# Kernel tuning notes

Hardware: AMD Instinct MI355X
Metric: run time of the kernel (lower is better)

## Reference

```python
import jax, jax.numpy as jnp
import numpy as np

NUM_HEADS = 16
HEAD_DIM = 80
HIDDEN = 1280
SEQ = 3072
NUM_SEGS = 6  # 6 packed images of 512 patches each


def rotate_half(x):
    x1, x2 = jnp.split(x, 2, axis=-1)
    return jnp.concatenate([-x2, x1], axis=-1)


def setup_inputs() -> dict:
    key = jax.random.key(0)
    ks = jax.random.split(key, 6)
    hidden_states = jax.random.normal(ks[0], (SEQ, HIDDEN), dtype=jnp.float32)
    # RoPE tables as in Qwen-VL vision: freqs over half the head_dim, duplicated
    half = HEAD_DIM // 2
    inv_freq = 1.0 / (10000.0 ** (jnp.arange(half, dtype=jnp.float32) / half))
    pos = jnp.arange(SEQ, dtype=jnp.float32)[:, None]
    freqs = pos * inv_freq[None, :]                      # (SEQ, half)
    emb = jnp.concatenate([freqs, freqs], axis=-1)       # (SEQ, HEAD_DIM)
    cos = jnp.cos(emb)
    sin = jnp.sin(emb)
    # Packed segment boundaries: [0, 512, 1024, ..., 3072]
    cu_seqlens = jnp.arange(0, SEQ + 1, SEQ // NUM_SEGS, dtype=jnp.int32)
    scale = 0.02
    w_qkv = jax.random.normal(ks[1], (3 * HIDDEN, HIDDEN), dtype=jnp.float32) * scale
    b_qkv = jax.random.normal(ks[2], (3 * HIDDEN,), dtype=jnp.float32) * scale
    w_proj = jax.random.normal(ks[3], (HIDDEN, HIDDEN), dtype=jnp.float32) * scale
    b_proj = jax.random.normal(ks[4], (HIDDEN,), dtype=jnp.float32) * scale
    return {
        "hidden_states": hidden_states, "cos": cos, "sin": sin,
        "w_qkv": w_qkv, "b_qkv": b_qkv, "w_proj": w_proj, "b_proj": b_proj,
        "cu_seqlens": cu_seqlens,
    }


def reference(hidden_states, cos, sin, w_qkv, b_qkv, w_proj, b_proj, cu_seqlens):
    S, H = hidden_states.shape
    nh, hd = NUM_HEADS, H // NUM_HEADS

    # Fused QKV projection: (S, 3H) -> q, k, v each (S, nh, hd)
    qkv = hidden_states @ w_qkv.T + b_qkv
    qkv = qkv.reshape(S, 3, nh, hd)
    q, k, v = qkv[:, 0], qkv[:, 1], qkv[:, 2]

    # Inline RoPE on q/k (cos/sin broadcast over heads)
    c = cos[:, None, :]
    s = sin[:, None, :]
    q = q * c + rotate_half(q) * s
    k = k * c + rotate_half(k) * s

    # Original casts fp32 -> fp16 for the flash attention kernel
    q16 = q.astype(jnp.float16)
    k16 = k.astype(jnp.float16)
    v16 = v.astype(jnp.float16)

    # Varlen masking: tokens attend only within their own packed segment
    tok = jnp.arange(S)
    seg = jnp.searchsorted(cu_seqlens, tok, side="right")  # (S,)
    same_seg = seg[:, None] == seg[None, :]                 # (S, S)

    scale = hd ** (-0.5)
    # Scores accumulated in fp32 (as flash attention does internally)
    scores = jnp.einsum("qhd,khd->hqk", q16, k16,
                        preferred_element_type=jnp.float32) * scale
    scores = jnp.where(same_seg[None], scores, jnp.finfo(jnp.float32).min)
    weights = jax.nn.softmax(scores, axis=-1).astype(jnp.float16)  # (nh, S, S)

    attn = jnp.einsum("hqk,khd->qhd", weights, v16)  # (S, nh, hd) fp16
    attn = attn.astype(jnp.float32).reshape(S, H)
    return attn @ w_proj.T + b_proj
```

## Files before the change

### kernel.cpp

```cpp
#include <hip/hip_runtime.h>

typedef _Float16 f16;
typedef _Float16 half8 __attribute__((ext_vector_type(8)));
typedef _Float16 half4 __attribute__((ext_vector_type(4)));
typedef float f32x4 __attribute__((ext_vector_type(4)));

__device__ __forceinline__ void gld_lds16(const void* g, void* l) {
  __builtin_amdgcn_global_load_lds((const __attribute__((address_space(1))) void*)g,
                                   (__attribute__((address_space(3))) void*)l, 16, 0, 0);
}

template <int CTRL>
__device__ __forceinline__ float dppf(float x) {
  return __builtin_bit_cast(float,
      __builtin_amdgcn_mov_dpp(__builtin_bit_cast(int, x), CTRL, 0xf, 0xf, true));
}
__device__ __forceinline__ float dpp_max16(float v) {
  v = fmaxf(v, dppf<0xB1>(v));
  v = fmaxf(v, dppf<0x4E>(v));
  v = fmaxf(v, dppf<0x128>(v));
  v = fmaxf(v, dppf<0x140>(v));
  return v;
}
__device__ __forceinline__ float dpp_sum16(float v) {
  v += dppf<0xB1>(v);
  v += dppf<0x4E>(v);
  v += dppf<0x128>(v);
  v += dppf<0x140>(v);
  return v;
}

__global__ void cvt_all(const float* __restrict__ hid, const float* __restrict__ wq,
                        const float* __restrict__ wp, f16* __restrict__ hid16,
                        f16* __restrict__ wq16, f16* __restrict__ wp16) {
  int b = blockIdx.x;
  const float* in;
  f16* out;
  int i;
  if (b < 3840) { in = hid; out = hid16; i = b * 256 + threadIdx.x; }
  else if (b < 8640) { in = wq; out = wq16; i = (b - 3840) * 256 + threadIdx.x; }
  else { in = wp; out = wp16; i = (b - 8640) * 256 + threadIdx.x; }
  float4 v = ((const float4*)in)[i];
  half4 o;
  o.x = (f16)v.x; o.y = (f16)v.y; o.z = (f16)v.z; o.w = (f16)v.w;
  ((half4*)out)[i] = o;
}

__global__ __launch_bounds__(512, 2) void gemm256(const f16* __restrict__ A,
                                                  const f16* __restrict__ B,
                                                  const float* __restrict__ bias,
                                                  f16* __restrict__ C) {
  __shared__ f16 S[65536];
  char* Sb = (char*)S;
  const int tid = threadIdx.x, lane = tid & 63, wid = tid >> 6;
  const int lm = lane & 15, q4 = lane >> 4;
  const int wm = wid >> 2, wn = wid & 3;
  const int bm = blockIdx.x * 256, bn = blockIdx.y * 256;
  const int w2 = wid * 2048;

  const int ch = ((lane & 7) ^ (lane >> 3)) << 3;
  const int r0 = wid * 16 + (lane >> 3);
  const int r1 = r0 + 8;
  uint32_t aoff[2][2], boff[2][2];
#pragma unroll
  for (int h = 0; h < 2; h++) {
    aoff[h][0] = (uint32_t)((bm + h * 64 + (r0 & 63) + ((r0 >> 6) << 7)) * 1280 + ch);
    aoff[h][1] = (uint32_t)((bm + h * 64 + (r1 & 63) + ((r1 >> 6) << 7)) * 1280 + ch);
    boff[h][0] = (uint32_t)((bn + h * 32 + (r0 & 31) + ((r0 >> 5) << 6)) * 1280 + ch);
    boff[h][1] = (uint32_t)((bn + h * 32 + (r1 & 31) + ((r1 >> 5) << 6)) * 1280 + ch);
  }

  int aro[4][2], bro[2][2];
#pragma unroll
  for (int f = 0; f < 4; f++)
#pragma unroll
    for (int ks = 0; ks < 2; ks++) {
      int row = wm * 64 + f * 16 + lm, colb = ks * 64 + q4 * 16;
      aro[f][ks] = row * 128 + (colb ^ ((row & 7) << 4));
    }
#pragma unroll
  for (int j = 0; j < 2; j++)
#pragma unroll
    for (int ks = 0; ks < 2; ks++) {
      int row = wn * 32 + j * 16 + lm, colb = ks * 64 + q4 * 16;
      bro[j][ks] = row * 128 + (colb ^ ((row & 7) << 4));
    }

  f32x4 acc[8][4] = {};

  {
    char* A0 = Sb;
    char* B0 = Sb + 65536;
    char* A1 = Sb + 32768;
    char* B1 = Sb + 98304;
    gld_lds16(A + aoff[0][0], A0 + w2);
    gld_lds16(A + aoff[0][1], A0 + w2 + 1024);
    gld_lds16(B + boff[1][0], B0 + 16384 + w2);
    gld_lds16(B + boff[1][1], B0 + 16384 + w2 + 1024);
    gld_lds16(A + aoff[1][0], A0 + 16384 + w2);
    gld_lds16(A + aoff[1][1], A0 + 16384 + w2 + 1024);
    gld_lds16(B + boff[0][0], B0 + w2);
    gld_lds16(B + boff[0][1], B0 + w2 + 1024);
    gld_lds16(A + aoff[0][0] + 64, A1 + w2);
    gld_lds16(A + aoff[0][1] + 64, A1 + w2 + 1024);
    gld_lds16(B + boff[1][0] + 64, B1 + 16384 + w2);
    gld_lds16(B + boff[1][1] + 64, B1 + 16384 + w2 + 1024);
    gld_lds16(A + aoff[1][0] + 64, A1 + 16384 + w2);
    gld_lds16(A + aoff[1][1] + 64, A1 + 16384 + w2 + 1024);
    asm volatile("s_waitcnt vmcnt(6)" ::: "memory");
    __builtin_amdgcn_s_barrier();
  }

  constexpr int NT = 20;
  half8 af[4][2], bf[2][2];
  for (int t = 0; t < NT; ++t) {
    const int p = t & 1;
    char* Ab = Sb + p * 32768;
    char* Bb = Sb + 65536 + p * 32768;
    char* Bn = Sb + 65536 + (p ^ 1) * 32768;
    const int k1 = (t + 1 < NT ? t + 1 : NT - 1) * 64;
    const int k2 = (t + 2 < NT ? t + 2 : NT - 1) * 64;

#pragma unroll
    for (int f = 0; f < 4; f++) {
      af[f][0] = *(const half8*)(Ab + aro[f][0]);
      af[f][1] = *(const half8*)(Ab + aro[f][1]);
    }
#pragma unroll
    for (int j = 0; j < 2; j++) {
      bf[j][0] = *(const half8*)(Bb + bro[j][0]);
      bf[j][1] = *(const half8*)(Bb + bro[j][1]);
    }
    gld_lds16(B + boff[0][0] + k1, Bn + w2);
    gld_lds16(B + boff[0][1] + k1, Bn + w2 + 1024);
    __builtin_amdgcn_s_barrier();
    asm volatile("s_waitcnt lgkmcnt(0)" ::: "memory");
    __builtin_amdgcn_sched_barrier(0);
    __builtin_amdgcn_s_setprio(1);
#pragma unroll
    for (int ks = 0; ks < 2; ks++)
#pragma unroll
      for (int f = 0; f < 4; f++)
#pragma unroll
        for (int j = 0; j < 2; j++)
          acc[f][j] =
              __builtin_amdgcn_mfma_f32_16x16x32_f16(af[f][ks], bf[j][ks], acc[f][j], 0, 0, 0);
    __builtin_amdgcn_s_setprio(0);
    __builtin_amdgcn_s_barrier();

#pragma unroll
    for (int j = 0; j < 2; j++) {
      bf[j][0] = *(const half8*)(Bb + 16384 + bro[j][0]);
      bf[j][1] = *(const half8*)(Bb + 16384 + bro[j][1]);
    }
    gld_lds16(A + aoff[0][0] + k2, Ab + w2);
    gld_lds16(A + aoff[0][1] + k2, Ab + w2 + 1024);
    __builtin_amdgcn_s_barrier();
    asm volatile("s_waitcnt lgkmcnt(0)" ::: "memory");
    __builtin_amdgcn_sched_barrier(0);
    __builtin_amdgcn_s_setprio(1);
#pragma unroll
    for (int ks = 0; ks < 2; ks++)
#pragma unroll
      for (int f = 0; f < 4; f++)
#pragma unroll
        for (int j = 0; j < 2; j++)
          acc[f][2 + j] =
              __builtin_amdgcn_mfma_f32_16x16x32_f16(af[f][ks], bf[j][ks], acc[f][2 + j], 0, 0, 0);
    __builtin_amdgcn_s_setprio(0);
    __builtin_amdgcn_s_barrier();

#pragma unroll
    for (int f = 0; f < 4; f++) {
      af[f][0] = *(const half8*)(Ab + 16384 + aro[f][0]);
      af[f][1] = *(const half8*)(Ab + 16384 + aro[f][1]);
    }
    gld_lds16(B + boff[1][0] + k2, Bb + 16384 + w2);
    gld_lds16(B + boff[1][1] + k2, Bb + 16384 + w2 + 1024);
    __builtin_amdgcn_s_barrier();
    asm volatile("s_waitcnt lgkmcnt(0)" ::: "memory");
    __builtin_amdgcn_sched_barrier(0);
    __builtin_amdgcn_s_setprio(1);
#pragma unroll
    for (int ks = 0; ks < 2; ks++)
#pragma unroll
      for (int f = 0; f < 4; f++)
#pragma unroll
        for (int j = 0; j < 2; j++)
          acc[4 + f][2 + j] = __builtin_amdgcn_mfma_f32_16x16x32_f16(af[f][ks], bf[j][ks],
                                                                     acc[4 + f][2 + j], 0, 0, 0);
    __builtin_amdgcn_s_setprio(0);
    __builtin_amdgcn_s_barrier();

#pragma unroll
    for (int j = 0; j < 2; j++) {
      bf[j][0] = *(const half8*)(Bb + bro[j][0]);
      bf[j][1] = *(const half8*)(Bb + bro[j][1]);
    }
    gld_lds16(A + aoff[1][0] + k2, Ab + 16384 + w2);
    gld_lds16(A + aoff[1][1] + k2, Ab + 16384 + w2 + 1024);
    asm volatile("s_waitcnt vmcnt(6)" ::: "memory");
    __builtin_amdgcn_s_barrier();
    asm volatile("s_waitcnt lgkmcnt(0)" ::: "memory");
    __builtin_amdgcn_sched_barrier(0);
    __builtin_amdgcn_s_setprio(1);
#pragma unroll
    for (int ks = 0; ks < 2; ks++)
#pragma unroll
      for (int f = 0; f < 4; f++)
#pragma unroll
        for (int j = 0; j < 2; j++)
          acc[4 + f][j] =
              __builtin_amdgcn_mfma_f32_16x16x32_f16(af[f][ks], bf[j][ks], acc[4 + f][j], 0, 0, 0);
    __builtin_amdgcn_s_setprio(0);
    __builtin_amdgcn_s_barrier();
  }

#pragma unroll
  for (int mf = 0; mf < 8; mf++)
#pragma unroll
    for (int nf = 0; nf < 4; nf++) {
      const int gc = bn + wn * 64 + nf * 16 + lm;
      const float bb = bias[gc];
      const int gr0 = bm + wm * 128 + mf * 16 + q4 * 4;
#pragma unroll
      for (int r = 0; r < 4; r++)
        C[(size_t)(gr0 + r) * 3840 + gc] = (f16)(acc[mf][nf][r] + bb);
    }
}

template <bool OUT_F16>
__global__ __launch_bounds__(256, 2) void gemm_bt64(const f16* __restrict__ A,
                                                    const f16* __restrict__ B,
                                                    const float* __restrict__ bias,
                                                    void* __restrict__ Cout,
                                                    int K, int lda, int ldb, int ldc) {
  __shared__ f16 As[64 * 32];
  __shared__ f16 Bs[128 * 32];
  const int tid = threadIdx.x, lane = tid & 63, wave = tid >> 6;
  const int bm = blockIdx.x * 64, bn = blockIdx.y * 128;
  const int wm = (wave & 1) * 32, wn = (wave >> 1) * 64;
  const int lm = lane & 15, kq = (lane >> 4) * 8;
  const int arow = tid >> 2, acol = (tid & 3) * 8;

  const f16* Ab = A + (size_t)(bm + arow) * lda + acol;
  const f16* Bb = B + (size_t)(bn + arow) * ldb + acol;
  f16* AsW = As + wave * 512;
  f16* BsW = Bs + wave * 512;

  f32x4 acc[2][4] = {};
  for (int k0 = 0; k0 < K; k0 += 32) {
    gld_lds16(Ab + k0, AsW);
    gld_lds16(Bb + k0, BsW);
    gld_lds16(Bb + (size_t)64 * ldb + k0, BsW + 2048);
    __syncthreads();
    half8 af[2], bf[4];
#pragma unroll
    for (int mt = 0; mt < 2; mt++) af[mt] = *(const half8*)&As[(wm + 16 * mt + lm) * 32 + kq];
#pragma unroll
    for (int nt = 0; nt < 4; nt++) bf[nt] = *(const half8*)&Bs[(wn + 16 * nt + lm) * 32 + kq];
#pragma unroll
    for (int mt = 0; mt < 2; mt++)
#pragma unroll
      for (int nt = 0; nt < 4; nt++)
        acc[mt][nt] = __builtin_amdgcn_mfma_f32_16x16x32_f16(af[mt], bf[nt], acc[mt][nt], 0, 0, 0);
    __syncthreads();
  }
  const int q4 = lane >> 4;
#pragma unroll
  for (int mt = 0; mt < 2; mt++)
#pragma unroll
    for (int nt = 0; nt < 4; nt++)
#pragma unroll
      for (int r = 0; r < 4; r++) {
        int gr = bm + wm + 16 * mt + 4 * q4 + r;
        int gc = bn + wn + 16 * nt + lm;
        float v = acc[mt][nt][r] + bias[gc];
        if (OUT_F16)
          ((f16*)Cout)[(size_t)gr * ldc + gc] = (f16)v;
        else
          ((float*)Cout)[(size_t)gr * ldc + gc] = v;
      }
}

__global__ void rope_transpose(f16* __restrict__ qkv, const float* __restrict__ cosb,
                               const float* __restrict__ sinb, f16* __restrict__ vt) {
  __shared__ f16 tile[64][72];
  const int b = blockIdx.x;
  if (b < 1920) {
    int idx = b * 256 + threadIdx.x;
    int c = idx % 5;
    int t = idx / 5;
    int h = t % 16; t /= 16;
    int qk = t & 1;
    int s = t >> 1;
    size_t base = (size_t)s * 3840 + qk * 1280 + h * 80 + c * 8;
    half8 x = *(half8*)&qkv[base];
    half8 y = *(half8*)&qkv[base + 40];
    const float* cp = cosb + s * 80 + c * 8;
    const float* sp = sinb + s * 80 + c * 8;
    half8 ox, oy;
#pragma unroll
    for (int i = 0; i < 8; i++) {
      float cs = cp[i], sn = sp[i];
      float xf = (float)x[i], yf = (float)y[i];
      ox[i] = (f16)(xf * cs - yf * sn);
      oy[i] = (f16)(yf * cs + xf * sn);
    }
    *(half8*)&qkv[base] = ox;
    *(half8*)&qkv[base + 40] = oy;
  } else {
    const int bb = b - 1920;
    const int bs = (bb % 48) * 64;
    const int bd = (bb / 48) * 64;
    const int r = threadIdx.x >> 2, c = (threadIdx.x & 3) * 16;
    *(uint4*)&tile[r][c] = *(const uint4*)&qkv[(size_t)(bs + r) * 3840 + 2560 + bd + c];
    *(uint4*)&tile[r][c + 8] = *(const uint4*)&qkv[(size_t)(bs + r) * 3840 + 2560 + bd + c + 8];
    __syncthreads();
    f16 tmp[16];
#pragma unroll
    for (int i = 0; i < 16; i++) tmp[i] = tile[c + i][r];
    *(uint4*)&vt[(size_t)(bd + r) * 3072 + bs + c] = *(uint4*)&tmp[0];
    *(uint4*)&vt[(size_t)(bd + r) * 3072 + bs + c + 8] = *(uint4*)&tmp[8];
  }
}

__global__ __launch_bounds__(256, 4) void flash_attn5(const f16* __restrict__ qkv,
                                                      const f16* __restrict__ vt,
                                                      f16* __restrict__ attn) {
  __shared__ f16 S[20480];
  f16* Ks = S;
  f16* Vs = S + 10240;
  const int tid = threadIdx.x, lane = tid & 63, wave = tid >> 6;
  const int lm = lane & 15, q4 = lane >> 4;
  const int h = blockIdx.x, g = blockIdx.z;
  const int qbase = g * 512 + blockIdx.y * 64 + wave * 16;
  f16* P = S + wave * 2112;
  const half8 hz = {};

  const f16* qrow = qkv + (size_t)(qbase + lm) * 3840 + h * 80;
  half8 qf[3];
  qf[0] = *(const half8*)(qrow + q4 * 8);
  qf[1] = *(const half8*)(qrow + 32 + q4 * 8);
  qf[2] = (q4 < 2) ? *(const half8*)(qrow + 64 + q4 * 8) : hz;

  size_t kgo[5], vgo[5];
#pragma unroll
  for (int i = 0; i < 5; i++) {
    int t = (wave * 5 + i) * 1024 + lane * 16;
    int kr = t / 160, kcb = t % 160;
    kgo[i] = (size_t)(g * 512 + kr) * 3840 + 1280 + h * 80 + (kcb >> 1);
    int vd = t >> 8, vsb = t & 255;
    vgo[i] = (size_t)(h * 80 + vd) * 3072 + g * 512 + (vsb >> 1);
  }

  f32x4 oacc[5] = {};
  float mprev[4] = {-1e30f, -1e30f, -1e30f, -1e30f};
  float lsum[4] = {0.f, 0.f, 0.f, 0.f};
  const float sc = 0.11180339887498949f * 1.4426950408889634f;

  for (int j = 0; j < 4; j++) {
    __syncthreads();
#pragma unroll
    for (int i = 0; i < 5; i++) {
      int chunk = wave * 5 + i;
      gld_lds16(qkv + kgo[i] + (size_t)j * (128 * 3840), Ks + chunk * 512);
      gld_lds16(vt + vgo[i] + j * 128, Vs + chunk * 512);
    }
    __syncthreads();

    f32x4 sacc[8] = {};
#pragma unroll
    for (int ks = 0; ks < 3; ks++) {
      half8 bk[8];
#pragma unroll
      for (int nt = 0; nt < 8; nt++)
        bk[nt] = (ks < 2 || q4 < 2)
                     ? *(const half8*)&Ks[(16 * nt + lm) * 80 + 32 * ks + q4 * 8]
                     : hz;
#pragma unroll
      for (int nt = 0; nt < 8; nt++)
        sacc[nt] = __builtin_amdgcn_mfma_f32_16x16x32_f16(qf[ks], bk[nt], sacc[nt], 0, 0, 0);
    }

    float mnew[4], alpha[4], rs[4];
#pragma unroll
    for (int r = 0; r < 4; r++) {
      float v = fmaxf(fmaxf(fmaxf(sacc[0][r], sacc[1][r]), fmaxf(sacc[2][r], sacc[3][r])),
                      fmaxf(fmaxf(sacc[4][r], sacc[5][r]), fmaxf(sacc[6][r], sacc[7][r])));
      v = dpp_max16(v);
      mnew[r] = fmaxf(mprev[r], v * sc);
      alpha[r] = __builtin_exp2f(mprev[r] - mnew[r]);
      mprev[r] = mnew[r];
      rs[r] = 0.f;
    }
#pragma unroll
    for (int nt = 0; nt < 8; nt++)
#pragma unroll
      for (int r = 0; r < 4; r++) {
        float p = __builtin_exp2f(sacc[nt][r] * sc - mnew[r]);
        sacc[nt][r] = p;
        rs[r] += p;
      }
#pragma unroll
    for (int r = 0; r < 4; r++) {
      float v = dpp_sum16(rs[r]);
      lsum[r] = alpha[r] * lsum[r] + v;
#pragma unroll
      for (int nt2 = 0; nt2 < 5; nt2++) oacc[nt2][r] *= alpha[r];
    }

    __syncthreads();
#pragma unroll
    for (int nt = 0; nt < 8; nt++)
#pragma unroll
      for (int r = 0; r < 4; r++)
        P[(4 * q4 + r) * 132 + 16 * nt + lm] = (f16)sacc[nt][r];

#pragma unroll
    for (int ks = 0; ks < 4; ks++) {
      half8 ap = *(const half8*)&P[lm * 132 + ks * 32 + q4 * 8];
      half8 bv[5];
#pragma unroll
      for (int nt2 = 0; nt2 < 5; nt2++)
        bv[nt2] = *(const half8*)&Vs[(16 * nt2 + lm) * 128 + ks * 32 + q4 * 8];
#pragma unroll
      for (int nt2 = 0; nt2 < 5; nt2++)
        oacc[nt2] = __builtin_amdgcn_mfma_f32_16x16x32_f16(ap, bv[nt2], oacc[nt2], 0, 0, 0);
    }
  }
#pragma unroll
  for (int r = 0; r < 4; r++) {
    float inv = 1.0f / lsum[r];
    int s = qbase + 4 * q4 + r;
#pragma unroll
    for (int nt2 = 0; nt2 < 5; nt2++)
      attn[(size_t)s * 1280 + h * 80 + 16 * nt2 + lm] = (f16)(oacc[nt2][r] * inv);
  }
}

extern "C" void kernel_launch(void* const* d_in, const int* in_sizes, int n_in,
                              void* d_out, int out_size, void* d_ws, size_t ws_size,
                              hipStream_t stream) {
  const float* hidden = (const float*)d_in[0];
  const float* cosb   = (const float*)d_in[1];
  const float* sinb   = (const float*)d_in[2];
  const float* w_qkv  = (const float*)d_in[3];
  const float* b_qkv  = (const float*)d_in[4];
  const float* w_proj = (const float*)d_in[5];
  const float* b_proj = (const float*)d_in[6];

  char* ws = (char*)d_ws;
  f16* hidden16 = (f16*)(ws + 0);
  f16* wqkv16   = (f16*)(ws + 7864320);
  f16* wproj16  = (f16*)(ws + 17694720);
  f16* qkv16    = (f16*)(ws + 20971520);
  f16* attn16   = (f16*)(ws + 44564480);
  f16* vt16     = hidden16;

  cvt_all<<<10240, 256, 0, stream>>>(hidden, w_qkv, w_proj, hidden16, wqkv16, wproj16);

  gemm256<<<dim3(12, 15), 512, 0, stream>>>(hidden16, wqkv16, b_qkv, qkv16);

  rope_transpose<<<2880, 256, 0, stream>>>(qkv16, cosb, sinb, vt16);

  flash_attn5<<<dim3(16, 8, 6), 256, 0, stream>>>(qkv16, vt16, attn16);

  gemm_bt64<false><<<dim3(48, 10), 256, 0, stream>>>(attn16, wproj16, b_proj, d_out,
                                                     1280, 1280, 1280, 1280);
}
```

Before: 213.1 us.

## Double-buffer K/V tiles in flash attention with 64-key blocks and swizzled V

The attention kernel now processes keys in blocks of 64 instead of 128 and keeps two LDS buffers. The next block is prefetched with global_load_lds while the current one is computed, so only one barrier is needed per iteration. Waves are split so two load K and two load V, and the V tile uses an XOR swizzle to cut LDS bank conflicts. The cost is more LDS per block and a lower occupancy hint (3 instead of 4), plus twice as many loop iterations with their softmax rescaling overhead.

```diff
diff --git a/kernel.cpp b/kernel.cpp
--- a/kernel.cpp
+++ b/kernel.cpp
@@ -325,17 +325,15 @@
   }
 }
 
-__global__ __launch_bounds__(256, 4) void flash_attn5(const f16* __restrict__ qkv,
+__global__ __launch_bounds__(256, 3) void flash_attn6(const f16* __restrict__ qkv,
                                                       const f16* __restrict__ vt,
                                                       f16* __restrict__ attn) {
-  __shared__ f16 S[20480];
-  f16* Ks = S;
-  f16* Vs = S + 10240;
+  __shared__ f16 S[25088];
   const int tid = threadIdx.x, lane = tid & 63, wave = tid >> 6;
   const int lm = lane & 15, q4 = lane >> 4;
   const int h = blockIdx.x, g = blockIdx.z;
   const int qbase = g * 512 + blockIdx.y * 64 + wave * 16;
-  f16* P = S + wave * 2112;
+  f16* P = S + 20480 + wave * 1152;
   const half8 hz = {};
 
   const f16* qrow = qkv + (size_t)(qbase + lm) * 3840 + h * 80;
@@ -344,14 +342,23 @@
   qf[1] = *(const half8*)(qrow + 32 + q4 * 8);
   qf[2] = (q4 < 2) ? *(const half8*)(qrow + 64 + q4 * 8) : hz;
 
-  size_t kgo[5], vgo[5];
+  const bool isK = wave < 2;
+  const f16* gsrc = isK ? qkv : vt;
+  const uint32_t gstep = isK ? (uint32_t)(64 * 3840) : 64u;
+  const int cbase = (wave & 1) * 5;
+  const uint32_t ldsoff = (isK ? 0u : 5120u) + (uint32_t)cbase * 512u;
+  uint32_t goff[5];
 #pragma unroll
   for (int i = 0; i < 5; i++) {
-    int t = (wave * 5 + i) * 1024 + lane * 16;
-    int kr = t / 160, kcb = t % 160;
-    kgo[i] = (size_t)(g * 512 + kr) * 3840 + 1280 + h * 80 + (kcb >> 1);
-    int vd = t >> 8, vsb = t & 255;
-    vgo[i] = (size_t)(h * 80 + vd) * 3072 + g * 512 + (vsb >> 1);
+    int t = (cbase + i) * 1024 + lane * 16;
+    if (isK) {
+      int row = t / 160, colb = t % 160;
+      goff[i] = (uint32_t)((g * 512 + row) * 3840 + 1280 + h * 80 + (colb >> 1));
+    } else {
+      int vd = t >> 7, vsb = t & 127;
+      int vsrc = vsb ^ ((vd & 7) << 4);
+      goff[i] = (uint32_t)((h * 80 + vd) * 3072 + g * 512 + (vsrc >> 1));
+    }
   }
 
   f32x4 oacc[5] = {};
@@ -359,35 +366,39 @@
   float lsum[4] = {0.f, 0.f, 0.f, 0.f};
   const float sc = 0.11180339887498949f * 1.4426950408889634f;
 
-  for (int j = 0; j < 4; j++) {
-    __syncthreads();
-#pragma unroll
-    for (int i = 0; i < 5; i++) {
-      int chunk = wave * 5 + i;
-      gld_lds16(qkv + kgo[i] + (size_t)j * (128 * 3840), Ks + chunk * 512);
-      gld_lds16(vt + vgo[i] + j * 128, Vs + chunk * 512);
-    }
-    __syncthreads();
-
-    f32x4 sacc[8] = {};
+#pragma unroll
+  for (int i = 0; i < 5; i++) gld_lds16(gsrc + goff[i], S + ldsoff + i * 512);
+  __syncthreads();
+
+  for (int jj = 0; jj < 8; jj++) {
+    const int p = jj & 1;
+    f16* Kb = S + p * 10240;
+    f16* Vb = Kb + 5120;
+    if (jj < 7) {
+#pragma unroll
+      for (int i = 0; i < 5; i++)
+        gld_lds16(gsrc + goff[i] + (uint32_t)(jj + 1) * gstep,
+                  S + (p ^ 1) * 10240 + ldsoff + i * 512);
+    }
+
+    f32x4 sacc[4] = {};
 #pragma unroll
     for (int ks = 0; ks < 3; ks++) {
-      half8 bk[8];
-#pragma unroll
-      for (int nt = 0; nt < 8; nt++)
+      half8 bk[4];
+#pragma unroll
+      for (int nt = 0; nt < 4; nt++)
         bk[nt] = (ks < 2 || q4 < 2)
-                     ? *(const half8*)&Ks[(16 * nt + lm) * 80 + 32 * ks + q4 * 8]
+                     ? *(const half8*)&Kb[(16 * nt + lm) * 80 + 32 * ks + q4 * 8]
                      : hz;
 #pragma unroll
-      for (int nt = 0; nt < 8; nt++)
+      for (int nt = 0; nt < 4; nt++)
         sacc[nt] = __builtin_amdgcn_mfma_f32_16x16x32_f16(qf[ks], bk[nt], sacc[nt], 0, 0, 0);
     }
 
     float mnew[4], alpha[4], rs[4];
 #pragma unroll
     for (int r = 0; r < 4; r++) {
-      float v = fmaxf(fmaxf(fmaxf(sacc[0][r], sacc[1][r]), fmaxf(sacc[2][r], sacc[3][r])),
-                      fmaxf(fmaxf(sacc[4][r], sacc[5][r]), fmaxf(sacc[6][r], sacc[7][r])));
+      float v = fmaxf(fmaxf(sacc[0][r], sacc[1][r]), fmaxf(sacc[2][r], sacc[3][r]));
       v = dpp_max16(v);
       mnew[r] = fmaxf(mprev[r], v * sc);
       alpha[r] = __builtin_exp2f(mprev[r] - mnew[r]);
@@ -395,12 +406,12 @@
       rs[r] = 0.f;
     }
 #pragma unroll
-    for (int nt = 0; nt < 8; nt++)
+    for (int nt = 0; nt < 4; nt++)
 #pragma unroll
       for (int r = 0; r < 4; r++) {
-        float p = __builtin_exp2f(sacc[nt][r] * sc - mnew[r]);
-        sacc[nt][r] = p;
-        rs[r] += p;
+        float pp = __builtin_exp2f(sacc[nt][r] * sc - mnew[r]);
+        sacc[nt][r] = pp;
+        rs[r] += pp;
       }
 #pragma unroll
     for (int r = 0; r < 4; r++) {
@@ -410,25 +421,29 @@
       for (int nt2 = 0; nt2 < 5; nt2++) oacc[nt2][r] *= alpha[r];
     }
 
-    __syncthreads();
-#pragma unroll
-    for (int nt = 0; nt < 8; nt++)
+#pragma unroll
+    for (int nt = 0; nt < 4; nt++)
 #pragma unroll
       for (int r = 0; r < 4; r++)
-        P[(4 * q4 + r) * 132 + 16 * nt + lm] = (f16)sacc[nt][r];
-
-#pragma unroll
-    for (int ks = 0; ks < 4; ks++) {
-      half8 ap = *(const half8*)&P[lm * 132 + ks * 32 + q4 * 8];
+        P[(4 * q4 + r) * 72 + 16 * nt + lm] = (f16)sacc[nt][r];
+
+#pragma unroll
+    for (int ks = 0; ks < 2; ks++) {
+      half8 ap = *(const half8*)&P[lm * 72 + ks * 32 + q4 * 8];
       half8 bv[5];
 #pragma unroll
-      for (int nt2 = 0; nt2 < 5; nt2++)
-        bv[nt2] = *(const half8*)&Vs[(16 * nt2 + lm) * 128 + ks * 32 + q4 * 8];
+      for (int nt2 = 0; nt2 < 5; nt2++) {
+        int row = 16 * nt2 + lm;
+        bv[nt2] = *(const half8*)&Vb[row * 64 + ((ks * 32 + q4 * 8) ^ ((row & 7) << 3))];
+      }
 #pragma unroll
       for (int nt2 = 0; nt2 < 5; nt2++)
         oacc[nt2] = __builtin_amdgcn_mfma_f32_16x16x32_f16(ap, bv[nt2], oacc[nt2], 0, 0, 0);
     }
-  }
+
+    __syncthreads();
+  }
+
 #pragma unroll
   for (int r = 0; r < 4; r++) {
     float inv = 1.0f / lsum[r];
@@ -464,7 +479,7 @@
 
   rope_transpose<<<2880, 256, 0, stream>>>(qkv16, cosb, sinb, vt16);
 
-  flash_attn5<<<dim3(16, 8, 6), 256, 0, stream>>>(qkv16, vt16, attn16);
+  flash_attn6<<<dim3(16, 8, 6), 256, 0, stream>>>(qkv16, vt16, attn16);
 
   gemm_bt64<false><<<dim3(48, 10), 256, 0, stream>>>(attn16, wproj16, b_proj, d_out,
                                                      1280, 1280, 1280, 1280);
```

Measured after the change: 194.3 us. 1.1x faster.
